# Performance work log

Hardware: AMD Instinct MI355X
Metric: run time of the kernel (lower is better)

The kernel has to match this reference:

```python
import jax, jax.numpy as jnp
import numpy as np

OVERLAP = 0.5
N_BOXES = 8192
FEATURE_LEN = 10


def _nms_keep(bboxes, scores, overlap):
    """Vectorized-equivalent of the sequential NMS while-loop.

    bboxes: [N,4] in (x, y, w, h) format (matches xmax = x + w in source).
    Returns a boolean keep mask over the original N boxes. Greedy order is
    descending score (source sorts ascending and pops the last element).
    Boxes with IoU > overlap w.r.t. a kept box are suppressed (iou.le(overlap)
    survives in the source).
    """
    N = bboxes.shape[0]
    x1 = bboxes[:, 0]
    y1 = bboxes[:, 1]
    x2 = bboxes[:, 0] + bboxes[:, 2]
    y2 = bboxes[:, 1] + bboxes[:, 3]
    area = (x2 - x1) * (y2 - y1)

    order = jnp.argsort(scores)[::-1]  # descending score
    xs1, ys1 = x1[order], y1[order]
    xs2, ys2 = x2[order], y2[order]
    ar = area[order]

    # Pairwise intersection in sorted order (same clamp math as the source).
    ix1 = jnp.maximum(xs1[:, None], xs1[None, :])
    iy1 = jnp.maximum(ys1[:, None], ys1[None, :])
    ix2 = jnp.minimum(xs2[:, None], xs2[None, :])
    iy2 = jnp.minimum(ys2[:, None], ys2[None, :])
    inter = jnp.clip(ix2 - ix1, 0.0) * jnp.clip(iy2 - iy1, 0.0)
    iou = inter / (ar[:, None] + ar[None, :] - inter)

    later = jnp.arange(N)[None, :] > jnp.arange(N)[:, None]
    sup = (iou > overlap) & later  # row i suppresses later j

    def body(i, state):
        keep, removed = state
        alive = jnp.logical_not(removed[i])
        keep = keep.at[i].set(alive)
        removed = removed | (alive & sup[i])
        return keep, removed

    keep_sorted, _ = jax.lax.fori_loop(
        0, N, body, (jnp.zeros(N, bool), jnp.zeros(N, bool)))
    # map back to original box indices
    return jnp.zeros(N, bool).at[order].set(keep_sorted)


def _bbox_regression(features, W, b, rect):
    """bounding_box_regression: t = sigmoid(Linear(features)); shift boxes."""
    t = jax.nn.sigmoid(features @ W + b)  # [N,4]
    x = jnp.clip(t[:, 0] * rect[:, 2] + rect[:, 0], 0.0)
    y = jnp.clip(t[:, 1] * rect[:, 3] + rect[:, 1], 0.0)
    w = rect[:, 2] * jnp.exp(t[:, 2])
    h = rect[:, 3] * jnp.exp(t[:, 3])
    return jnp.stack([x, y, w, h], axis=-1)


def setup_inputs() -> dict:
    key = jax.random.key(0)
    k0, k1, k2, k3, k4 = jax.random.split(key, 5)
    N = N_BOXES
    bboxes = jax.random.uniform(k0, (N, 4), jnp.float32)  # (x,y,w,h) in [0,1)
    scores = jax.random.uniform(k1, (N,), jnp.float32)
    features = jax.random.normal(k2, (N, FEATURE_LEN), jnp.float32)
    W = jax.random.normal(k3, (FEATURE_LEN, 4), jnp.float32) * 0.1
    b = jax.random.normal(k4, (4,), jnp.float32) * 0.1
    return {"bboxes": bboxes, "scores": scores, "features": features,
            "W": W, "b": b, "width": 1024, "height": 1024}


def reference(bboxes, scores, features, W, b, width, height):
    keep = _nms_keep(bboxes, scores, OVERLAP)
    reg = _bbox_regression(features, W, b, bboxes)
    # transform_bounding_box with start_points=(0,0), scales=(1,1):
    # scales normalized coords back to pixel space.
    scale = jnp.array([width, height, width, height], jnp.float32)
    out = reg * scale * keep[:, None].astype(reg.dtype)
    return out
```

## Files before the change

kernel.cpp:

```cpp
#include <hip/hip_runtime.h>
#include <hip/hip_bf16.h>

#define N_BOXES 8192
#define NW 128
#define NREG 64
#define FEAT 10
#define NSLOT 4

typedef unsigned long long u64;
typedef unsigned int u32;

__device__ __forceinline__ void barrier_nodrain() {
    asm volatile("s_waitcnt lgkmcnt(0)" ::: "memory");
    __builtin_amdgcn_sched_barrier(0);
    __builtin_amdgcn_s_barrier();
    __builtin_amdgcn_sched_barrier(0);
    asm volatile("" ::: "memory");
}

__global__ void rank_scatter_kernel(const float* __restrict__ bboxes,
                                    const float* __restrict__ scores,
                                    float* __restrict__ x1s, float* __restrict__ y1s,
                                    float* __restrict__ x2s, float* __restrict__ y2s,
                                    u32* __restrict__ rank_of) {
    __shared__ float sc[N_BOXES];
    int tid = threadIdx.x;
    for (int t = 0; t < N_BOXES / 256; ++t)
        sc[tid + 256 * t] = scores[tid + 256 * t];
    __syncthreads();
    int k = tid >> 3;
    int s = tid & 7;
    int i = blockIdx.x * 32 + k;
    float si = sc[i];
    int cnt = 0;
    const float4* sc4 = (const float4*)sc;
    int q0 = s * (N_BOXES / 32);
    #pragma unroll 4
    for (int q = q0; q < q0 + N_BOXES / 32; ++q) {
        float4 v = sc4[q];
        int j = 4 * q;
        cnt += (int)((v.x > si) || (v.x == si && j     > i));
        cnt += (int)((v.y > si) || (v.y == si && j + 1 > i));
        cnt += (int)((v.z > si) || (v.z == si && j + 2 > i));
        cnt += (int)((v.w > si) || (v.w == si && j + 3 > i));
    }
    cnt += __shfl_down(cnt, 4, 8);
    cnt += __shfl_down(cnt, 2, 8);
    cnt += __shfl_down(cnt, 1, 8);
    if (s == 0) {
        int r = cnt;
        float x = bboxes[4 * i + 0], y = bboxes[4 * i + 1];
        float w = bboxes[4 * i + 2], h = bboxes[4 * i + 3];
        float x2 = x + w, y2 = y + h;
        x1s[r] = x; y1s[r] = y; x2s[r] = x2; y2s[r] = y2;
        rank_of[i] = (u32)r;
    }
}

__global__ void __launch_bounds__(256) mask_kernel(
        const float* __restrict__ x1s, const float* __restrict__ y1s,
        const float* __restrict__ x2s, const float* __restrict__ y2s,
        u64* __restrict__ RM, u64* __restrict__ TRb) {
    int wv = threadIdx.x >> 6, lane = threadIdx.x & 63;
    int ci = blockIdx.x;
    int cj = blockIdx.y * 4 + wv;
    if (cj < ci) return;
    __shared__ float S[4][4][64];
    int d = cj - ci;
    int ig0 = ci * 64, jg0 = cj * 64;
    if (d <= 5) {
        S[wv][0][lane] = x1s[ig0 + lane];
        S[wv][1][lane] = y1s[ig0 + lane];
        S[wv][2][lane] = x2s[ig0 + lane];
        S[wv][3][lane] = y2s[ig0 + lane];
        int jg = jg0 + lane;
        float jx1 = x1s[jg], jy1 = y1s[jg], jx2 = x2s[jg], jy2 = y2s[jg];
        float jar = (jx2 - jx1) * (jy2 - jy1);
        u64 my = 0, cw = 0;
        for (int ip = 0; ip < 64; ++ip) {
            float ax1 = S[wv][0][ip], ay1 = S[wv][1][ip];
            float ax2 = S[wv][2][ip], ay2 = S[wv][3][ip];
            float aar = (ax2 - ax1) * (ay2 - ay1);
            float xx1 = fmaxf(ax1, jx1);
            float yy1 = fmaxf(ay1, jy1);
            float xx2 = fminf(ax2, jx2);
            float yy2 = fminf(ay2, jy2);
            float iw = fmaxf(xx2 - xx1, 0.0f);
            float ih = fmaxf(yy2 - yy1, 0.0f);
            float inter = iw * ih;
            float uni = aar + jar - inter;
            float iou = __fdiv_rn(inter, uni);
            bool sup = (iou > 0.5f) && (jg > ig0 + ip);
            u64 w = __ballot(sup);
            if (lane == ip) my = w;
            cw |= sup ? (1ull << ip) : 0ull;
        }
        RM[(size_t)(ig0 + lane) * NW + cj] = my;
        TRb[(size_t)d * N_BOXES + jg] = cw;
    } else {
        S[wv][0][lane] = x1s[jg0 + lane];
        S[wv][1][lane] = y1s[jg0 + lane];
        S[wv][2][lane] = x2s[jg0 + lane];
        S[wv][3][lane] = y2s[jg0 + lane];
        int ig = ig0 + lane;
        float ix1 = x1s[ig], iy1 = y1s[ig], ix2 = x2s[ig], iy2 = y2s[ig];
        float iar = (ix2 - ix1) * (iy2 - iy1);
        u64 my = 0;
        for (int jp = 0; jp < 64; ++jp) {
            float jx1 = S[wv][0][jp], jy1 = S[wv][1][jp];
            float jx2 = S[wv][2][jp], jy2 = S[wv][3][jp];
            float jar = (jx2 - jx1) * (jy2 - jy1);
            float xx1 = fmaxf(ix1, jx1);
            float yy1 = fmaxf(iy1, jy1);
            float xx2 = fminf(ix2, jx2);
            float yy2 = fminf(iy2, jy2);
            float iw = fmaxf(xx2 - xx1, 0.0f);
            float ih = fmaxf(yy2 - yy1, 0.0f);
            float inter = iw * ih;
            float uni = iar + jar - inter;
            float iou = __fdiv_rn(inter, uni);
            bool sup = (iou > 0.5f);
            my |= sup ? (1ull << jp) : 0ull;
        }
        RM[(size_t)ig * NW + cj] = my;
    }
}

__global__ void __launch_bounds__(512) nms_reduce(
        const u64* __restrict__ RM, const u64* __restrict__ TRb,
        u64* __restrict__ keepw_g) {
    __shared__ __align__(8) u32 rem32[NW * 2];
    __shared__ u64 keptw[NW];
    __shared__ unsigned char klA[4][64], klB[4][64];

    const int tid = threadIdx.x;
    const int wv = tid >> 6, lane = tid & 63;
    const int grp = wv - 1;

    if (tid < NW * 2) rem32[tid] = 0;

    u64 TDe[2], T1e[2], T2e[2], T3e[2], T4e[2];
    u64 TDo[2], T1o[2], T2o[2], T3o[2], T4o[2], T5o[2];
    u64 kp1 = 0, kp2 = 0, kp3 = 0, kp4 = 0;
    if (wv == 0) {
        TDe[0] = TRb[lane];
        T1e[0] = TRb[N_BOXES + lane];
        T2e[0] = TRb[2 * N_BOXES + lane];
        T3e[0] = TRb[3 * N_BOXES + lane];
        T4e[0] = TRb[4 * N_BOXES + lane];
        TDo[0] = TRb[64 + lane];
        T1o[0] = TRb[N_BOXES + 64 + lane];
        T2o[0] = TRb[2 * N_BOXES + 64 + lane];
        T3o[0] = TRb[3 * N_BOXES + 64 + lane];
        T4o[0] = TRb[4 * N_BOXES + 64 + lane];
        T5o[0] = TRb[5 * N_BOXES + 64 + lane];
    }
    u64 HA0[NSLOT], HA1[NSLOT], HB0[NSLOT], HB1[NSLOT];
    u32 KnA = 0, KnB = 0;
    __syncthreads();

#define FIXPOINT(TD, RIN, KOUT)                                                 \
    {                                                                           \
      u64 K = 0, U = ~(RIN);                                                    \
      bool meU = (U >> lane) & 1;                                               \
      while (U) {                                                               \
        u64 UK = U | K;                                                         \
        u64 nK = __ballot(meU && (((TD) & UK) == 0ull));                        \
        K |= nK;                                                                \
        u64 nR = __ballot(meU && (((TD) & K) != 0ull));                         \
        U &= ~(K | nR);                                                         \
        meU = (U >> lane) & 1;                                                  \
      }                                                                         \
      (KOUT) = K;                                                               \
    }

#define REGION(Q, PAR)                                                          \
  do {                                                                          \
    const int q_ = (Q);                                                         \
    const int c0 = 2 * q_, c1 = 2 * q_ + 1;                                     \
    if (wv == 0) {                                                              \
      if (q_ + 1 < NREG) {                   \
        const int n0 = (c0 + 2) * 64 + lane, n1 = n0 + 64;                      \
        TDe[PAR ^ 1] = TRb[n0];                                                 \
        T1e[PAR ^ 1] = TRb[N_BOXES + n0];                                       \
        T2e[PAR ^ 1] = TRb[2 * N_BOXES + n0];                                   \
        T3e[PAR ^ 1] = TRb[3 * N_BOXES + n0];                                   \
        T4e[PAR ^ 1] = TRb[4 * N_BOXES + n0];                                   \
        TDo[PAR ^ 1] = TRb[n1];                                                 \
        T1o[PAR ^ 1] = TRb[N_BOXES + n1];                                       \
        T2o[PAR ^ 1] = TRb[2 * N_BOXES + n1];                                   \
        T3o[PAR ^ 1] = TRb[3 * N_BOXES + n1];                                   \
        T4o[PAR ^ 1] = TRb[4 * N_BOXES + n1];                                   \
        T5o[PAR ^ 1] = TRb[5 * N_BOXES + n1];                                   \
      }                                                                         \
      u64 K0, K1;                                                               \
      {                                                                         \
        u64 base0 = *(const u64*)&rem32[2 * c0];                                \
        u64 R0 = base0 | __ballot(((T1e[PAR] & kp1) | (T2e[PAR] & kp2) |        \
                                   (T3e[PAR] & kp3) | (T4e[PAR] & kp4)) != 0ull);\
        FIXPOINT(TDe[PAR], R0, K0);                                             \
        bool isk = (K0 >> lane) & 1;                                            \
        int rnk = __popcll(K0 & ((1ull << lane) - 1ull));                       \
        if (isk) klA[q_ & 3][rnk] = (unsigned char)lane;                        \
        if (lane == 0) keptw[c0] = K0;                                          \
      }                                                                         \
      {                                                                         \
        u64 base1 = *(const u64*)&rem32[2 * c1];                                \
        u64 R1 = base1 | __ballot(((T1o[PAR] & K0)  | (T2o[PAR] & kp1) |        \
                                   (T3o[PAR] & kp2) | (T4o[PAR] & kp3) |        \
                                   (T5o[PAR] & kp4)) != 0ull);                  \
        FIXPOINT(TDo[PAR], R1, K1);                                             \
        bool isk = (K1 >> lane) & 1;                                            \
        int rnk = __popcll(K1 & ((1ull << lane) - 1ull));                       \
        if (isk) klB[q_ & 3][rnk] = (unsigned char)lane;                        \
        if (lane == 0) keptw[c1] = K1;                                          \
      }                                                                         \
      kp4 = kp2; kp3 = kp1; kp2 = K0; kp1 = K1;                                 \
    } else {                                                                    \
                      \
      if (q_ >= 2 && (KnA | KnB)) {                                             \
        const int wd0 = 2 * q_ + 1 + lane;                                      \
        const int wd1 = wd0 + 64;                                               \
        u64 v0 = 0, v1 = 0;                                                     \
        _Pragma("unroll")                                                       \
        for (int s = 0; s < NSLOT; ++s) {                                       \
          v0 |= HA0[s] | HB0[s];                                                \
          v1 |= HA1[s] | HB1[s];                                                \
        }                                                                       \
        if (KnA > 7u * NSLOT) {                              \
          const u32 cpb = (u32)(2 * q_ - 4) * 64u;                              \
          const unsigned char* kl = klA[(q_ - 2) & 3];                          \
          for (u32 r = 7u * NSLOT + (u32)grp; r < KnA; r += 7u) {               \
            const u64* rp = RM + (size_t)(cpb + kl[r]) * NW;                    \
            if (wd0 < NW) v0 |= rp[wd0];                                        \
            if (wd1 < NW) v1 |= rp[wd1];                                        \
          }                                                                     \
        }                                                                       \
        if (KnB > 7u * NSLOT) {                                                 \
          const u32 cpb = (u32)(2 * q_ - 3) * 64u;                              \
          const unsigned char* kl = klB[(q_ - 2) & 3];                          \
          for (u32 r = 7u * NSLOT + (u32)grp; r < KnB; r += 7u) {               \
            const u64* rp = RM + (size_t)(cpb + kl[r]) * NW;                    \
            if (wd0 < NW) v0 |= rp[wd0];                                        \
            if (wd1 < NW) v1 |= rp[wd1];                                        \
          }                                                                     \
        }                                                                       \
        if (wd0 < NW && v0) atomicOr((u64*)&rem32[2 * wd0], v0);                \
        if (wd1 < NW && v1) atomicOr((u64*)&rem32[2 * wd1], v1);                \
      }                                                                         \
                    \
      {                                                                         \
        const int ib = 2 * q_ + 3;                                              \
        if (q_ >= 1 && ib < NW) {                                               \
          const u32 cA = (u32)(2 * q_ - 2) * 64u, cB = cA + 64u;                \
          KnA = (u32)__popcll(keptw[2 * q_ - 2]);                               \
          KnB = (u32)__popcll(keptw[2 * q_ - 1]);                               \
          const int wi0 = ib + lane;                                            \
          const int wi1 = wi0 + 64;                                             \
          const unsigned char* kla = klA[(q_ - 1) & 3];                         \
          const unsigned char* klb = klB[(q_ - 1) & 3];                         \
          _Pragma("unroll")                                                     \
          for (int s = 0; s < NSLOT; ++s) {                                     \
            HA0[s] = 0; HA1[s] = 0; HB0[s] = 0; HB1[s] = 0;                     \
            u32 r = (u32)(s * 7 + grp);                       \
            if (r < KnA) {                                                      \
              const u64* rp = RM + (size_t)(cA + kla[r]) * NW;                  \
              if (wi0 < NW) HA0[s] = rp[wi0];                                   \
              if (wi1 < NW) HA1[s] = rp[wi1];                                   \
            }                                                                   \
            if (r < KnB) {                                                      \
              const u64* rp = RM + (size_t)(cB + klb[r]) * NW;                  \
              if (wi0 < NW) HB0[s] = rp[wi0];                                   \
              if (wi1 < NW) HB1[s] = rp[wi1];                                   \
            }                                                                   \
          }                                                                     \
        } else { KnA = 0; KnB = 0; }                                            \
      }                                                                         \
    }                                                                           \
    barrier_nodrain();                                                          \
  } while (0)

    for (int qq = 0; qq < NREG; qq += 2) {
        REGION(qq, 0);
        REGION(qq + 1, 1);
    }
#undef REGION
#undef FIXPOINT

    __syncthreads();
    if (tid < NW) keepw_g[tid] = keptw[tid];
}

__global__ void output_kernel(const float* __restrict__ bboxes,
                              const float* __restrict__ features,
                              const float* __restrict__ Wm, const float* __restrict__ bv,
                              const int* __restrict__ widthp, const int* __restrict__ heightp,
                              const u32* __restrict__ rank_of, const u64* __restrict__ keepw,
                              float* __restrict__ out) {
    int i = blockIdx.x * blockDim.x + threadIdx.x;
    if (i >= N_BOXES) return;
    u32 r = rank_of[i];
    float keep = (float)((keepw[r >> 6] >> (r & 63)) & 1ull);
    float z0 = bv[0], z1 = bv[1], z2 = bv[2], z3 = bv[3];
    #pragma unroll
    for (int m = 0; m < FEAT; ++m) {
        float f = features[i * FEAT + m];
        z0 += f * Wm[m * 4 + 0];
        z1 += f * Wm[m * 4 + 1];
        z2 += f * Wm[m * 4 + 2];
        z3 += f * Wm[m * 4 + 3];
    }
    float t0 = 1.0f / (1.0f + expf(-z0));
    float t1 = 1.0f / (1.0f + expf(-z1));
    float t2 = 1.0f / (1.0f + expf(-z2));
    float t3 = 1.0f / (1.0f + expf(-z3));
    float4 bx = ((const float4*)bboxes)[i];
    float ox = fmaxf(t0 * bx.z + bx.x, 0.0f);
    float oy = fmaxf(t1 * bx.w + bx.y, 0.0f);
    float ow = bx.z * expf(t2);
    float oh = bx.w * expf(t3);
    float sw = (float)(*widthp), sh = (float)(*heightp);
    float4 o;
    o.x = ox * sw * keep;
    o.y = oy * sh * keep;
    o.z = ow * sw * keep;
    o.w = oh * sh * keep;
    ((float4*)out)[i] = o;
}

extern "C" void kernel_launch(void* const* d_in, const int* in_sizes, int n_in,
                              void* d_out, int out_size, void* d_ws, size_t ws_size,
                              hipStream_t stream) {
    const float* bboxes   = (const float*)d_in[0];
    const float* scores   = (const float*)d_in[1];
    const float* features = (const float*)d_in[2];
    const float* Wm       = (const float*)d_in[3];
    const float* bv       = (const float*)d_in[4];
    const int*   widthp   = (const int*)d_in[5];
    const int*   heightp  = (const int*)d_in[6];
    float* out = (float*)d_out;

    char* ws = (char*)d_ws;
    u64* RM      = (u64*)ws;
    u64* TRb     = (u64*)(ws + (size_t)N_BOXES * NW * sizeof(u64));
    float* x1s   = (float*)((char*)TRb + (size_t)6 * N_BOXES * sizeof(u64));
    float* y1s   = x1s + N_BOXES;
    float* x2s   = y1s + N_BOXES;
    float* y2s   = x2s + N_BOXES;
    u32* rank_of = (u32*)(y2s + N_BOXES);
    u64* keepw   = (u64*)(rank_of + N_BOXES);

    rank_scatter_kernel<<<N_BOXES / 32, 256, 0, stream>>>(bboxes, scores,
                                                          x1s, y1s, x2s, y2s, rank_of);
    mask_kernel<<<dim3(NW, NW / 4), 256, 0, stream>>>(x1s, y1s, x2s, y2s, RM, TRb);
    nms_reduce<<<1, 512, 0, stream>>>(RM, TRb, keepw);
    output_kernel<<<N_BOXES / 256, 256, 0, stream>>>(bboxes, features, Wm, bv,
                                                     widthp, heightp, rank_of, keepw, out);
}
```

Before: 131.3 us.

## Shrink NMS reduce block to 256 threads with per-wave word ownership

Reduces the single-block serial NMS reduction from 8 waves to 4. Two helper waves each own 64 mask words instead of seven waves splitting kept rows round-robin, and the prefetch depth doubles to 8 rows per kept list. The rem32 base loads are hoisted ahead of the next-region prefetch in the leader wave. The aim is cheaper barriers and less cross-wave atomic contention, but each helper wave now walks every kept row serially, so dense regions may take longer.

```diff
diff --git a/kernel.cpp b/kernel.cpp
--- a/kernel.cpp
+++ b/kernel.cpp
@@ -5,7 +5,7 @@
 #define NW 128
 #define NREG 64
 #define FEAT 10
-#define NSLOT 4
+#define NSLOT 8
 
 typedef unsigned long long u64;
 typedef unsigned int u32;
@@ -126,7 +126,7 @@
     }
 }
 
-__global__ void __launch_bounds__(512) nms_reduce(
+__global__ void __launch_bounds__(256) nms_reduce(
         const u64* __restrict__ RM, const u64* __restrict__ TRb,
         u64* __restrict__ keepw_g) {
     __shared__ __align__(8) u32 rem32[NW * 2];
@@ -135,9 +135,8 @@
 
     const int tid = threadIdx.x;
     const int wv = tid >> 6, lane = tid & 63;
-    const int grp = wv - 1;
-
-    if (tid < NW * 2) rem32[tid] = 0;
+
+    rem32[tid] = 0;
 
     u64 TDe[2], T1e[2], T2e[2], T3e[2], T4e[2];
     u64 TDo[2], T1o[2], T2o[2], T3o[2], T4o[2], T5o[2];
@@ -155,7 +154,9 @@
         T4o[0] = TRb[4 * N_BOXES + 64 + lane];
         T5o[0] = TRb[5 * N_BOXES + 64 + lane];
     }
-    u64 HA0[NSLOT], HA1[NSLOT], HB0[NSLOT], HB1[NSLOT];
+    u64 HA[NSLOT], HB[NSLOT];
+    #pragma unroll
+    for (int s = 0; s < NSLOT; ++s) { HA[s] = 0; HB[s] = 0; }
     u32 KnA = 0, KnB = 0;
     __syncthreads();
 
@@ -179,6 +180,9 @@
     const int q_ = (Q);                                                         \
     const int c0 = 2 * q_, c1 = 2 * q_ + 1;                                     \
     if (wv == 0) {                                                              \
+             \
+      u64 base0 = *(const u64*)&rem32[2 * c0];                                  \
+      u64 base1 = *(const u64*)&rem32[2 * c1];                                  \
       if (q_ + 1 < NREG) {                   \
         const int n0 = (c0 + 2) * 64 + lane, n1 = n0 + 64;                      \
         TDe[PAR ^ 1] = TRb[n0];                                                 \
@@ -195,7 +199,6 @@
       }                                                                         \
       u64 K0, K1;                                                               \
       {                                                                         \
-        u64 base0 = *(const u64*)&rem32[2 * c0];                                \
         u64 R0 = base0 | __ballot(((T1e[PAR] & kp1) | (T2e[PAR] & kp2) |        \
                                    (T3e[PAR] & kp3) | (T4e[PAR] & kp4)) != 0ull);\
         FIXPOINT(TDe[PAR], R0, K0);                                             \
@@ -205,7 +208,6 @@
         if (lane == 0) keptw[c0] = K0;                                          \
       }                                                                         \
       {                                                                         \
-        u64 base1 = *(const u64*)&rem32[2 * c1];                                \
         u64 R1 = base1 | __ballot(((T1o[PAR] & K0)  | (T2o[PAR] & kp1) |        \
                                    (T3o[PAR] & kp2) | (T4o[PAR] & kp3) |        \
                                    (T5o[PAR] & kp4)) != 0ull);                  \
@@ -216,37 +218,26 @@
         if (lane == 0) keptw[c1] = K1;                                          \
       }                                                                         \
       kp4 = kp2; kp3 = kp1; kp2 = K0; kp1 = K1;                                 \
-    } else {                                                                    \
-                      \
+    } else if (wv <= 2) {                                                       \
+                 \
       if (q_ >= 2 && (KnA | KnB)) {                                             \
-        const int wd0 = 2 * q_ + 1 + lane;                                      \
-        const int wd1 = wd0 + 64;                                               \
-        u64 v0 = 0, v1 = 0;                                                     \
+        const int wd = 2 * q_ + 1 + lane + (wv - 1) * 64;                       \
+        u64 v = 0;                                                              \
         _Pragma("unroll")                                                       \
-        for (int s = 0; s < NSLOT; ++s) {                                       \
-          v0 |= HA0[s] | HB0[s];                                                \
-          v1 |= HA1[s] | HB1[s];                                                \
-        }                                                                       \
-        if (KnA > 7u * NSLOT) {                              \
+        for (int s = 0; s < NSLOT; ++s) v |= HA[s] | HB[s];                     \
+        if (KnA > (u32)NSLOT && wd < NW) {                   \
           const u32 cpb = (u32)(2 * q_ - 4) * 64u;                              \
           const unsigned char* kl = klA[(q_ - 2) & 3];                          \
-          for (u32 r = 7u * NSLOT + (u32)grp; r < KnA; r += 7u) {               \
-            const u64* rp = RM + (size_t)(cpb + kl[r]) * NW;                    \
-            if (wd0 < NW) v0 |= rp[wd0];                                        \
-            if (wd1 < NW) v1 |= rp[wd1];                                        \
-          }                                                                     \
+          for (u32 r = (u32)NSLOT; r < KnA; ++r)                                \
+            v |= RM[(size_t)(cpb + kl[r]) * NW + wd];                           \
         }                                                                       \
-        if (KnB > 7u * NSLOT) {                                                 \
+        if (KnB > (u32)NSLOT && wd < NW) {                                      \
           const u32 cpb = (u32)(2 * q_ - 3) * 64u;                              \
           const unsigned char* kl = klB[(q_ - 2) & 3];                          \
-          for (u32 r = 7u * NSLOT + (u32)grp; r < KnB; r += 7u) {               \
-            const u64* rp = RM + (size_t)(cpb + kl[r]) * NW;                    \
-            if (wd0 < NW) v0 |= rp[wd0];                                        \
-            if (wd1 < NW) v1 |= rp[wd1];                                        \
-          }                                                                     \
+          for (u32 r = (u32)NSLOT; r < KnB; ++r)                                \
+            v |= RM[(size_t)(cpb + kl[r]) * NW + wd];                           \
         }                                                                       \
-        if (wd0 < NW && v0) atomicOr((u64*)&rem32[2 * wd0], v0);                \
-        if (wd1 < NW && v1) atomicOr((u64*)&rem32[2 * wd1], v1);                \
+        if (wd < NW && v) atomicOr((u64*)&rem32[2 * wd], v);                    \
       }                                                                         \
                     \
       {                                                                         \
@@ -255,24 +246,16 @@
           const u32 cA = (u32)(2 * q_ - 2) * 64u, cB = cA + 64u;                \
           KnA = (u32)__popcll(keptw[2 * q_ - 2]);                               \
           KnB = (u32)__popcll(keptw[2 * q_ - 1]);                               \
-          const int wi0 = ib + lane;                                            \
-          const int wi1 = wi0 + 64;                                             \
+          const int wi = ib + lane + (wv - 1) * 64;                             \
           const unsigned char* kla = klA[(q_ - 1) & 3];                         \
           const unsigned char* klb = klB[(q_ - 1) & 3];                         \
           _Pragma("unroll")                                                     \
           for (int s = 0; s < NSLOT; ++s) {                                     \
-            HA0[s] = 0; HA1[s] = 0; HB0[s] = 0; HB1[s] = 0;                     \
-            u32 r = (u32)(s * 7 + grp);                       \
-            if (r < KnA) {                                                      \
-              const u64* rp = RM + (size_t)(cA + kla[r]) * NW;                  \
-              if (wi0 < NW) HA0[s] = rp[wi0];                                   \
-              if (wi1 < NW) HA1[s] = rp[wi1];                                   \
-            }                                                                   \
-            if (r < KnB) {                                                      \
-              const u64* rp = RM + (size_t)(cB + klb[r]) * NW;                  \
-              if (wi0 < NW) HB0[s] = rp[wi0];                                   \
-              if (wi1 < NW) HB1[s] = rp[wi1];                                   \
-            }                                                                   \
+            HA[s] = 0; HB[s] = 0;                                               \
+            if ((u32)s < KnA && wi < NW)                                        \
+              HA[s] = RM[(size_t)(cA + kla[s]) * NW + wi];                      \
+            if ((u32)s < KnB && wi < NW)                                        \
+              HB[s] = RM[(size_t)(cB + klb[s]) * NW + wi];                      \
           }                                                                     \
         } else { KnA = 0; KnB = 0; }                                            \
       }                                                                         \
@@ -353,7 +336,7 @@
     rank_scatter_kernel<<<N_BOXES / 32, 256, 0, stream>>>(bboxes, scores,
                                                           x1s, y1s, x2s, y2s, rank_of);
     mask_kernel<<<dim3(NW, NW / 4), 256, 0, stream>>>(x1s, y1s, x2s, y2s, RM, TRb);
-    nms_reduce<<<1, 512, 0, stream>>>(RM, TRb, keepw);
+    nms_reduce<<<1, 256, 0, stream>>>(RM, TRb, keepw);
     output_kernel<<<N_BOXES / 256, 256, 0, stream>>>(bboxes, features, Wm, bv,
                                                      widthp, heightp, rank_of, keepw, out);
 }
```

After: 266.7 us. +103.2%, slower.
